# Performance work log

Measured on AMD Instinct MI355X. Metric: run time of the kernel, lower is better.

Reference implementation:

```python
import jax, jax.numpy as jnp
import numpy as np


def _gcn_norm(edge_index, num_nodes):
    # PyG GCNConv: add self-loops, symmetric normalization D^-1/2 (A+I) D^-1/2
    src, dst = edge_index[0], edge_index[1]
    loop = jnp.arange(num_nodes, dtype=edge_index.dtype)
    src = jnp.concatenate([src, loop])
    dst = jnp.concatenate([dst, loop])
    deg = jnp.zeros((num_nodes,), jnp.float32).at[dst].add(1.0)
    dinv = jnp.where(deg > 0, jax.lax.rsqrt(deg), 0.0)
    norm = dinv[src] * dinv[dst]  # [E + N]
    return src, dst, norm


def _gcn_conv(x, src, dst, norm, W, b):
    h = x @ W                                    # [N, out] dense GEMM first
    msg = h[src] * norm[:, None]                  # gather + scale, [E+N, out]
    agg = jax.ops.segment_sum(msg, dst, num_segments=x.shape[0])
    return agg + b


def setup_inputs() -> dict:
    key = jax.random.key(0)
    ks = jax.random.split(key, 8)
    N, E, F, H1, H2, C = 100000, 1600000, 128, 128, 128, 40
    s = 1.0 / np.sqrt(F)
    return {
        "x": jax.random.normal(ks[0], (N, F), jnp.float32),
        "edge_index": jax.random.randint(ks[1], (2, E), 0, N, jnp.int64),
        "W1": jax.random.normal(ks[2], (F, H1), jnp.float32) * s,
        "b1": jnp.zeros((H1,), jnp.float32),
        "W2": jax.random.normal(ks[3], (H1, H2), jnp.float32) * s,
        "b2": jnp.zeros((H2,), jnp.float32),
        "W3": jax.random.normal(ks[4], (H2, C), jnp.float32) * s,
        "b3": jnp.zeros((C,), jnp.float32),
    }


def reference(x, edge_index, W1, b1, W2, b2, W3, b3):
    N = x.shape[0]
    src, dst, norm = _gcn_norm(edge_index, N)
    h = jax.nn.relu(_gcn_conv(x, src, dst, norm, W1, b1))  # dropout is identity in eval
    h = jax.nn.relu(_gcn_conv(h, src, dst, norm, W2, b2))
    h = _gcn_conv(h, src, dst, norm, W3, b3)
    return jax.nn.log_softmax(h, axis=1)
```

## Files before the change

kernel.cpp:

```cpp
#include <hip/hip_runtime.h>
#include <hip/hip_bf16.h>
#include <math.h>

typedef short bf16x8 __attribute__((ext_vector_type(8)));
typedef unsigned short us8 __attribute__((ext_vector_type(8)));
typedef float f32x4 __attribute__((ext_vector_type(4)));

__device__ __forceinline__ float bf2f(unsigned short u) {
    return __uint_as_float(((unsigned)u) << 16);
}
__device__ __forceinline__ unsigned short f2bf(float f) {
    unsigned u = __float_as_uint(f);
    return (unsigned short)((u + 0x7FFF + ((u >> 16) & 1)) >> 16);
}

__global__ void ell_scatter(const int* __restrict__ ei, int* __restrict__ cnt,
                            int* __restrict__ ell, int E) {
    int e = blockIdx.x * blockDim.x + threadIdx.x;
    if (e < E) {
        int s = ei[e], d = ei[E + e];
        int idx = atomicAdd(&cnt[d], 1);
        if (idx < 64) ell[(d << 6) + idx] = s;
    }
}

__global__ void dinv_kernel(const int* __restrict__ cnt, float* __restrict__ dinv, int N) {
    int v = blockIdx.x * blockDim.x + threadIdx.x;
    if (v < N) dinv[v] = rsqrtf((float)(cnt[v] + 1));
}

struct TW {
    const float* src[3];
    unsigned short* dst[3];
    int C[3];
};
__global__ __launch_bounds__(256) void transposeW(TW tw) {
    __shared__ float Ts[128 * 128];
    int b = blockIdx.x;
    const float* W = tw.src[b];
    unsigned short* WT = tw.dst[b];
    int C = tw.C[b];
    int t = threadIdx.x;
    for (int i = t; i < 128 * C; i += 256) Ts[i] = W[i];
    __syncthreads();
    for (int i = t; i < C * 128; i += 256) {
        int c = i >> 7, k = i & 127;
        WT[c * 128 + k] = f2bf(Ts[k * C + c]);
    }
}

template<int NT, int NCOL, bool FP32IN>
__global__ __launch_bounds__(256) void gemm_mfma(const void* __restrict__ Xin,
                                                 const unsigned short* __restrict__ WT,
                                                 const float* __restrict__ dinv,
                                                 unsigned short* __restrict__ Hout, int N) {
    __shared__ unsigned short Ws[NT * 16 * 128];
    __shared__ unsigned short Xs[64 * 128];
    int t = threadIdx.x;
    int row0 = blockIdx.x * 64;
    for (int i = t; i < NT * 16 * 16; i += 256) {
        int r = i >> 4, s = i & 15;
        us8 val = (us8)0;
        if (r < NCOL) val = *(const us8*)&WT[r * 128 + s * 8];
        int byte = (r * 256) + ((s * 16) ^ ((r & 7) << 4));
        *(us8*)((char*)Ws + byte) = val;
    }
    for (int i = t; i < 64 * 16; i += 256) {
        int r = i >> 4, s = i & 15;
        int gr = row0 + r;
        us8 val = (us8)0;
        if (gr < N) {
            if (FP32IN) {
                const float4* Xf = (const float4*)Xin;
                float4 f0 = Xf[(size_t)gr * 32 + s * 2];
                float4 f1 = Xf[(size_t)gr * 32 + s * 2 + 1];
                val[0] = f2bf(f0.x); val[1] = f2bf(f0.y); val[2] = f2bf(f0.z); val[3] = f2bf(f0.w);
                val[4] = f2bf(f1.x); val[5] = f2bf(f1.y); val[6] = f2bf(f1.z); val[7] = f2bf(f1.w);
            } else {
                const unsigned short* Xh = (const unsigned short*)Xin;
                val = *(const us8*)&Xh[(size_t)gr * 128 + s * 8];
            }
        }
        int byte = (r * 256) + ((s * 16) ^ ((r & 7) << 4));
        *(us8*)((char*)Xs + byte) = val;
    }
    __syncthreads();

    int wid = t >> 6, lane = t & 63;
    int arow = wid * 16 + (lane & 15);
    f32x4 acc[NT];
#pragma unroll
    for (int i = 0; i < NT; i++) acc[i] = 0.0f;

#pragma unroll
    for (int kk = 0; kk < 4; kk++) {
        int kbyte = kk * 64 + (lane >> 4) * 16;
        bf16x8 a = *(const bf16x8*)((const char*)Xs + (arow * 256) + (kbyte ^ ((arow & 7) << 4)));
#pragma unroll
        for (int ct = 0; ct < NT; ct++) {
            int brow = ct * 16 + (lane & 15);
            bf16x8 b = *(const bf16x8*)((const char*)Ws + (brow * 256) + (kbyte ^ ((brow & 7) << 4)));
            acc[ct] = __builtin_amdgcn_mfma_f32_16x16x32_bf16(a, b, acc[ct], 0, 0, 0);
        }
    }
    int dcol = lane & 15;
    int drow = wid * 16 + (lane >> 4) * 4;
#pragma unroll
    for (int ct = 0; ct < NT; ct++) {
        int col = ct * 16 + dcol;
#pragma unroll
        for (int j = 0; j < 4; j++) {
            int grow = row0 + drow + j;
            if (grow < N && col < NCOL)
                Hout[(size_t)grow * NCOL + col] = f2bf(acc[ct][j] * dinv[grow]);
        }
    }
}

__global__ __launch_bounds__(256) void agg128_b(const ushort4* __restrict__ Hp,
                                                const int* __restrict__ cnt,
                                                const int* __restrict__ ell,
                                                const float* __restrict__ dinv,
                                                const float* __restrict__ bias,
                                                ushort4* __restrict__ Hout, int N) {
    int r = blockIdx.x * 8 + (threadIdx.x >> 5);
    if (r >= N) return;
    int lane = threadIdx.x & 31;
    int deg = min(cnt[r], 64);
    const int* nb = &ell[r << 6];
    ushort4 sv = Hp[(size_t)r * 32 + lane];
    float a0 = bf2f(sv.x), a1 = bf2f(sv.y), a2 = bf2f(sv.z), a3 = bf2f(sv.w);
    int p = 0;
    for (; p + 8 <= deg; p += 8) {
        int s0 = nb[p + 0], s1 = nb[p + 1], s2 = nb[p + 2], s3 = nb[p + 3];
        int s4 = nb[p + 4], s5 = nb[p + 5], s6 = nb[p + 6], s7 = nb[p + 7];
        ushort4 v0 = Hp[(size_t)s0 * 32 + lane];
        ushort4 v1 = Hp[(size_t)s1 * 32 + lane];
        ushort4 v2 = Hp[(size_t)s2 * 32 + lane];
        ushort4 v3 = Hp[(size_t)s3 * 32 + lane];
        ushort4 v4 = Hp[(size_t)s4 * 32 + lane];
        ushort4 v5 = Hp[(size_t)s5 * 32 + lane];
        ushort4 v6 = Hp[(size_t)s6 * 32 + lane];
        ushort4 v7 = Hp[(size_t)s7 * 32 + lane];
        a0 += bf2f(v0.x) + bf2f(v1.x) + bf2f(v2.x) + bf2f(v3.x)
            + bf2f(v4.x) + bf2f(v5.x) + bf2f(v6.x) + bf2f(v7.x);
        a1 += bf2f(v0.y) + bf2f(v1.y) + bf2f(v2.y) + bf2f(v3.y)
            + bf2f(v4.y) + bf2f(v5.y) + bf2f(v6.y) + bf2f(v7.y);
        a2 += bf2f(v0.z) + bf2f(v1.z) + bf2f(v2.z) + bf2f(v3.z)
            + bf2f(v4.z) + bf2f(v5.z) + bf2f(v6.z) + bf2f(v7.z);
        a3 += bf2f(v0.w) + bf2f(v1.w) + bf2f(v2.w) + bf2f(v3.w)
            + bf2f(v4.w) + bf2f(v5.w) + bf2f(v6.w) + bf2f(v7.w);
    }
    for (; p < deg; ++p) {
        int s = nb[p];
        ushort4 v = Hp[(size_t)s * 32 + lane];
        a0 += bf2f(v.x); a1 += bf2f(v.y); a2 += bf2f(v.z); a3 += bf2f(v.w);
    }
    float dv = dinv[r];
    float o0 = fmaxf(a0 * dv + bias[lane * 4 + 0], 0.f);
    float o1 = fmaxf(a1 * dv + bias[lane * 4 + 1], 0.f);
    float o2 = fmaxf(a2 * dv + bias[lane * 4 + 2], 0.f);
    float o3 = fmaxf(a3 * dv + bias[lane * 4 + 3], 0.f);
    ushort4 o; o.x = f2bf(o0); o.y = f2bf(o1); o.z = f2bf(o2); o.w = f2bf(o3);
    Hout[(size_t)r * 32 + lane] = o;
}

__global__ __launch_bounds__(256) void agg40_lsm(const ushort4* __restrict__ Gs,
                                                 const int* __restrict__ cnt,
                                                 const int* __restrict__ ell,
                                                 const float* __restrict__ dinv,
                                                 const float* __restrict__ b3,
                                                 float* __restrict__ Out, int N) {
    int t = threadIdx.x;
    int wv = t >> 6;
    int lw = t & 63;
    int g = lw / 10;
    int l = lw - g * 10;
    if (g >= 6) return;
    int r = blockIdx.x * 24 + wv * 6 + g;
    if (r >= N) return;
    int deg = min(cnt[r], 64);
    const int* nb = &ell[r << 6];
    ushort4 sv = Gs[(size_t)r * 10 + l];
    float a0 = bf2f(sv.x), a1 = bf2f(sv.y), a2 = bf2f(sv.z), a3 = bf2f(sv.w);
    int p = 0;
    for (; p + 4 <= deg; p += 4) {
        int s0 = nb[p], s1 = nb[p + 1], s2 = nb[p + 2], s3 = nb[p + 3];
        ushort4 v0 = Gs[(size_t)s0 * 10 + l];
        ushort4 v1 = Gs[(size_t)s1 * 10 + l];
        ushort4 v2 = Gs[(size_t)s2 * 10 + l];
        ushort4 v3 = Gs[(size_t)s3 * 10 + l];
        a0 += bf2f(v0.x) + bf2f(v1.x) + bf2f(v2.x) + bf2f(v3.x);
        a1 += bf2f(v0.y) + bf2f(v1.y) + bf2f(v2.y) + bf2f(v3.y);
        a2 += bf2f(v0.z) + bf2f(v1.z) + bf2f(v2.z) + bf2f(v3.z);
        a3 += bf2f(v0.w) + bf2f(v1.w) + bf2f(v2.w) + bf2f(v3.w);
    }
    for (; p < deg; ++p) {
        int s = nb[p];
        ushort4 v = Gs[(size_t)s * 10 + l];
        a0 += bf2f(v.x); a1 += bf2f(v.y); a2 += bf2f(v.z); a3 += bf2f(v.w);
    }
    float dv = dinv[r];
    float v0 = a0 * dv + b3[4 * l + 0];
    float v1 = a1 * dv + b3[4 * l + 1];
    float v2 = a2 * dv + b3[4 * l + 2];
    float v3 = a3 * dv + b3[4 * l + 3];
    float m4 = fmaxf(fmaxf(v0, v1), fmaxf(v2, v3));
    float m = m4;
#pragma unroll
    for (int k = 1; k < 10; k++)
        m = fmaxf(m, __shfl(m4, g * 10 + ((l + k) % 10), 64));
    float e4 = expf(v0 - m) + expf(v1 - m) + expf(v2 - m) + expf(v3 - m);
    float ssum = e4;
#pragma unroll
    for (int k = 1; k < 10; k++)
        ssum += __shfl(e4, g * 10 + ((l + k) % 10), 64);
    float lse = m + logf(ssum);
    float4 o = make_float4(v0 - lse, v1 - lse, v2 - lse, v3 - lse);
    *(float4*)&Out[(size_t)r * 40 + 4 * l] = o;
}

extern "C" void kernel_launch(void* const* d_in, const int* in_sizes, int n_in,
                              void* d_out, int out_size, void* d_ws, size_t ws_size,
                              hipStream_t stream) {
    const float* x  = (const float*)d_in[0];
    const int*   ei = (const int*)d_in[1];
    const float* W1 = (const float*)d_in[2];
    const float* b1 = (const float*)d_in[3];
    const float* W2 = (const float*)d_in[4];
    const float* b2 = (const float*)d_in[5];
    const float* W3 = (const float*)d_in[6];
    const float* b3 = (const float*)d_in[7];
    float* out = (float*)d_out;

    const int N = in_sizes[0] / 128;
    const int E = in_sizes[1] / 2;

    auto align = [](size_t v) { return (v + 255) & ~(size_t)255; };
    char* w = (char*)d_ws;
    size_t off = 0;
    unsigned short* bufA = (unsigned short*)(w + off); off += align((size_t)N * 128 * 2);
    unsigned short* bufB = (unsigned short*)(w + off); off += align((size_t)N * 128 * 2);
    unsigned short* gs   = (unsigned short*)(w + off); off += align((size_t)N * 40 * 2);
    unsigned short* W1T  = (unsigned short*)(w + off); off += align(128 * 128 * 2);
    unsigned short* W2T  = (unsigned short*)(w + off); off += align(128 * 128 * 2);
    unsigned short* W3T  = (unsigned short*)(w + off); off += align(40 * 128 * 2);
    int* cnt  = (int*)(w + off);   off += align((size_t)N * 4);
    float* dinv = (float*)(w + off); off += align((size_t)N * 4);
    int* ell  = (int*)(w + off);   off += align((size_t)N * 64 * 4);

    hipMemsetAsync(cnt, 0, (size_t)N * 4, stream);

    TW tw;
    tw.src[0] = W1; tw.dst[0] = W1T; tw.C[0] = 128;
    tw.src[1] = W2; tw.dst[1] = W2T; tw.C[1] = 128;
    tw.src[2] = W3; tw.dst[2] = W3T; tw.C[2] = 40;
    transposeW<<<3, 256, 0, stream>>>(tw);

    ell_scatter<<<(E + 255) / 256, 256, 0, stream>>>(ei, cnt, ell, E);
    dinv_kernel<<<(N + 255) / 256, 256, 0, stream>>>(cnt, dinv, N);

    int ggemm = (N + 63) / 64;
    int gagg  = (N + 7) / 8;
    gemm_mfma<8, 128, true><<<ggemm, 256, 0, stream>>>(x, W1T, dinv, bufA, N);
    agg128_b<<<gagg, 256, 0, stream>>>((const ushort4*)bufA, cnt, ell, dinv, b1,
                                       (ushort4*)bufB, N);
    gemm_mfma<8, 128, false><<<ggemm, 256, 0, stream>>>(bufB, W2T, dinv, bufA, N);
    agg128_b<<<gagg, 256, 0, stream>>>((const ushort4*)bufA, cnt, ell, dinv, b2,
                                       (ushort4*)bufB, N);
    gemm_mfma<3, 40, false><<<ggemm, 256, 0, stream>>>(bufB, W3T, dinv, gs, N);
    agg40_lsm<<<(N + 23) / 24, 256, 0, stream>>>((const ushort4*)gs, cnt, ell, dinv,
                                                 b3, out, N);
}
```

Before: 472.3 us.

## Partition ELL build by XCC to localize degree atomics, then compact

Edge scatter now reads the hardware XCC id and keeps separate per-XCC degree counters and 8-slot ELL buckets, so the atomics and stores stay within one die's L2 instead of contending across chiplets. Edges that overflow a bucket go to the tail of the final ELL row through a second atomic counter. A new compact kernel uses an 8-lane prefix scan to merge the per-XCC buckets and the overflow entries into the final 64-wide ELL, and it also computes degree and dinv, which replaces the old dinv kernel. In exchange it adds a larger memset, an extra pass over the adjacency data, and reuse of the activation buffers as scratch space.

```diff
diff --git a/kernel.cpp b/kernel.cpp
--- a/kernel.cpp
+++ b/kernel.cpp
@@ -14,19 +14,58 @@
     return (unsigned short)((u + 0x7FFF + ((u >> 16) & 1)) >> 16);
 }
 
-__global__ void ell_scatter(const int* __restrict__ ei, int* __restrict__ cnt,
-                            int* __restrict__ ell, int E) {
+__global__ void ell2_scatter(const int* __restrict__ ei, int* __restrict__ cnt8,
+                             int* __restrict__ ovfcnt, int* __restrict__ ell2,
+                             int* __restrict__ ellf, int N, int E) {
+    unsigned x;
+    asm volatile("s_getreg_b32 %0, hwreg(HW_REG_XCC_ID)" : "=s"(x));
+    x &= 7;
     int e = blockIdx.x * blockDim.x + threadIdx.x;
-    if (e < E) {
-        int s = ei[e], d = ei[E + e];
-        int idx = atomicAdd(&cnt[d], 1);
-        if (idx < 64) ell[(d << 6) + idx] = s;
-    }
-}
-
-__global__ void dinv_kernel(const int* __restrict__ cnt, float* __restrict__ dinv, int N) {
-    int v = blockIdx.x * blockDim.x + threadIdx.x;
-    if (v < N) dinv[v] = rsqrtf((float)(cnt[v] + 1));
+    if (e >= E) return;
+    int s = ei[e], d = ei[E + e];
+    int idx = atomicAdd(&cnt8[x * N + d], 1);
+    if (idx < 8) {
+        ell2[((size_t)x * N + d) * 8 + idx] = s;
+    } else {
+        int oi = atomicAdd(&ovfcnt[d], 1);
+        ellf[(d << 6) + 63 - oi] = s;
+    }
+}
+
+__global__ __launch_bounds__(256) void compact(const int* __restrict__ cnt8,
+                                               const int* __restrict__ ovfcnt,
+                                               const int* __restrict__ ell2,
+                                               int* __restrict__ ellf,
+                                               int* __restrict__ cnt,
+                                               float* __restrict__ dinv, int N) {
+    int t = threadIdx.x;
+    int g = t >> 3;
+    int x = t & 7;
+    int d = blockIdx.x * 32 + g;
+    if (d >= N) return;
+    int k = cnt8[x * N + d];
+    int kc = min(k, 8);
+    int pre = kc;
+#pragma unroll
+    for (int sh = 1; sh < 8; sh <<= 1) {
+        int v = __shfl_up(pre, sh, 8);
+        if (x >= sh) pre += v;
+    }
+    int off = pre - kc;
+    int tot = __shfl(pre, 7, 8);
+    for (int i = 0; i < kc; i++)
+        ellf[(d << 6) + off + i] = ell2[((size_t)x * N + d) * 8 + i];
+    int oc = ovfcnt[d];
+    int vbuf[8];
+    int nv = 0;
+    for (int i = x; i < oc; i += 8) vbuf[nv++] = ellf[(d << 6) + 63 - i];
+    int k2 = 0;
+    for (int i = x; i < oc; i += 8) ellf[(d << 6) + tot + i] = vbuf[k2++];
+    if (x == 0) {
+        int deg = tot + oc;
+        cnt[d] = deg;
+        dinv[d] = rsqrtf((float)(deg + 1));
+    }
 }
 
 struct TW {
@@ -247,9 +286,13 @@
     unsigned short* W3T  = (unsigned short*)(w + off); off += align(40 * 128 * 2);
     int* cnt  = (int*)(w + off);   off += align((size_t)N * 4);
     float* dinv = (float*)(w + off); off += align((size_t)N * 4);
-    int* ell  = (int*)(w + off);   off += align((size_t)N * 64 * 4);
-
-    hipMemsetAsync(cnt, 0, (size_t)N * 4, stream);
+    int* ellf = (int*)(w + off);   off += align((size_t)N * 64 * 4);
+
+    int* ell2   = (int*)bufA;
+    int* cnt8   = (int*)gs;
+    int* ovfcnt = cnt8 + 8 * (size_t)N;
+
+    hipMemsetAsync(cnt8, 0, (size_t)9 * N * 4, stream);
 
     TW tw;
     tw.src[0] = W1; tw.dst[0] = W1T; tw.C[0] = 128;
@@ -257,18 +300,18 @@
     tw.src[2] = W3; tw.dst[2] = W3T; tw.C[2] = 40;
     transposeW<<<3, 256, 0, stream>>>(tw);
 
-    ell_scatter<<<(E + 255) / 256, 256, 0, stream>>>(ei, cnt, ell, E);
-    dinv_kernel<<<(N + 255) / 256, 256, 0, stream>>>(cnt, dinv, N);
+    ell2_scatter<<<(E + 255) / 256, 256, 0, stream>>>(ei, cnt8, ovfcnt, ell2, ellf, N, E);
+    compact<<<(N + 31) / 32, 256, 0, stream>>>(cnt8, ovfcnt, ell2, ellf, cnt, dinv, N);
 
     int ggemm = (N + 63) / 64;
     int gagg  = (N + 7) / 8;
     gemm_mfma<8, 128, true><<<ggemm, 256, 0, stream>>>(x, W1T, dinv, bufA, N);
-    agg128_b<<<gagg, 256, 0, stream>>>((const ushort4*)bufA, cnt, ell, dinv, b1,
+    agg128_b<<<gagg, 256, 0, stream>>>((const ushort4*)bufA, cnt, ellf, dinv, b1,
                                        (ushort4*)bufB, N);
     gemm_mfma<8, 128, false><<<ggemm, 256, 0, stream>>>(bufB, W2T, dinv, bufA, N);
-    agg128_b<<<gagg, 256, 0, stream>>>((const ushort4*)bufA, cnt, ell, dinv, b2,
+    agg128_b<<<gagg, 256, 0, stream>>>((const ushort4*)bufA, cnt, ellf, dinv, b2,
                                        (ushort4*)bufB, N);
     gemm_mfma<3, 40, false><<<ggemm, 256, 0, stream>>>(bufB, W3T, dinv, gs, N);
-    agg40_lsm<<<(N + 23) / 24, 256, 0, stream>>>((const ushort4*)gs, cnt, ell, dinv,
+    agg40_lsm<<<(N + 23) / 24, 256, 0, stream>>>((const ushort4*)gs, cnt, ellf, dinv,
                                                  b3, out, N);
 }
```

Measured after the change: 477.3 us. No clear change (+1.1%).
